# Performance work log

Measured on AMD Instinct MI355X. Metric: run time of the kernel, lower is better.

The kernel has to match this reference:

```python
import jax, jax.numpy as jnp
import numpy as np

NUM_EMB = 512
DIM = 65        # so dim-1 = 64 Householder reflections of size 64x64 per embedding
B, N = 2048, 256


def setup_inputs() -> dict:
    key = jax.random.key(0)
    k1, k2, k3, k4 = jax.random.split(key, 4)
    x = jax.random.normal(k1, (B, N, DIM), dtype=jnp.float32)
    r_idx = jax.random.randint(k2, (B,), 0, NUM_EMB)
    # learned params: embedding table and scalar flip_sign (nn.Parameter)
    emb_weight = jax.random.normal(k3, (NUM_EMB, (DIM - 1) * (DIM - 1)), dtype=jnp.float32)
    flip_sign = jax.random.normal(k4, (), dtype=jnp.float32)
    return {"x": x, "r_idx": r_idx, "emb_weight": emb_weight, "flip_sign": flip_sign}


def _flg_forward(x, emb_weight, flip_sign, r_idx):
    d = DIM - 1
    # GELU (exact, matching torch default) then view as [E, d, d]; row w is a reflection vector v
    v = jax.nn.gelu(emb_weight, approximate=False).reshape(NUM_EMB, d, d)
    # Householder matrices H[e, w] = I - 2 v v^T / (v . v)   -> [E, d, d, d]
    outer = jnp.einsum('ewv,ewk->ewvk', v, v)
    sqnorm = jnp.einsum('ewv,ewv->ew', v, v)[..., None, None]
    H = jnp.eye(d, dtype=x.dtype) - 2.0 * outer / sqnorm
    H = jnp.transpose(H, (1, 0, 2, 3))  # [d, E, d, d]: reflection index leading (scan axis)

    # sequential product W = I @ H[0] @ H[1] @ ... @ H[d-1], batched over E
    W0 = jnp.broadcast_to(jnp.eye(d, dtype=x.dtype), (NUM_EMB, d, d))
    def step(carry, Hi):
        return carry @ Hi, None
    W, _ = jax.lax.scan(step, W0, H)  # [E, d, d]

    # scale last column by flip_sign (in-place mul in torch)
    W = W.at[:, :, -1].multiply(flip_sign)

    Wb = W[r_idx]                        # [B, d, d]
    x0 = x[..., :1]                      # [B, N, 1]
    xn = jnp.einsum('bnd,bdc->bnc', x[..., 1:], Wb)  # rotate remaining coords
    return jnp.concatenate([x0, xn], axis=-1)


def reference(x, r_idx, emb_weight, flip_sign):
    xo = _flg_forward(x, emb_weight, flip_sign, r_idx)
    return (xo, r_idx)
```

## Files before the change

### kernel.cpp

```cpp
#include <hip/hip_runtime.h>
#include <math.h>

#define NUM_EMB 512
#define DIMV 65
#define DD   64
#define BB   2048
#define NN   256
#define IMGF (16 * DIMV)

typedef short short8 __attribute__((ext_vector_type(8)));
typedef float f32x4  __attribute__((ext_vector_type(4)));
typedef float f4u    __attribute__((ext_vector_type(4), aligned(4)));

__device__ __forceinline__ float gelu_exact(float x) {
    return 0.5f * x * (1.0f + erff(x * 0.7071067811865475f));
}

__device__ __forceinline__ unsigned f2bf_u(float f) {
    unsigned u = __builtin_bit_cast(unsigned, f);
    u += 0x7FFFu + ((u >> 16) & 1u);
    return u >> 16;
}
__device__ __forceinline__ unsigned short f2bf(float f) {
    return (unsigned short)f2bf_u(f);
}

__global__ __launch_bounds__(256) void build_W(const float* __restrict__ emb,
                                               const float* __restrict__ flip_sign,
                                               const int*   __restrict__ r_idx,
                                               unsigned short* __restrict__ WgT,
                                               float* __restrict__ out) {
    __shared__ float v_lds[DD * DD];
    __shared__ float s_lds[DD];
    const int e = blockIdx.x;
    const int t = threadIdx.x;
    const int r = t >> 2;
    const int q = t & 3;

    const float* erow = emb + (size_t)e * (DD * DD);
    #pragma unroll
    for (int p = 0; p < 16; ++p) {
        int idx = p * 256 + t;
        v_lds[idx] = gelu_exact(erow[idx]);
    }

    if (t < 4) {
        int bi = e * 4 + t;
        out[(size_t)BB * NN * DIMV + bi] = (float)r_idx[bi];
    }
    __syncthreads();

    {
        const float* vr = &v_lds[r * DD + q * 16];
        float ss = 0.f;
        #pragma unroll
        for (int k = 0; k < 16; ++k) ss += vr[k] * vr[k];
        ss += __shfl_xor(ss, 1);
        ss += __shfl_xor(ss, 2);
        if (q == 0) s_lds[r] = 2.0f / ss;
    }
    __syncthreads();

    float Wq[16];
    #pragma unroll
    for (int k = 0; k < 16; ++k) Wq[k] = ((q * 16 + k) == r) ? 1.0f : 0.0f;

    float vv[16], nv[16];
    {
        const float* vr = &v_lds[q * 16];
        *(float4*)&nv[0]  = *(const float4*)&vr[0];
        *(float4*)&nv[4]  = *(const float4*)&vr[4];
        *(float4*)&nv[8]  = *(const float4*)&vr[8];
        *(float4*)&nv[12] = *(const float4*)&vr[12];
    }

    for (int w = 0; w < DD; ++w) {
        #pragma unroll
        for (int k = 0; k < 16; ++k) vv[k] = nv[k];
        if (w < DD - 1) {
            const float* vr = &v_lds[(w + 1) * DD + q * 16];
            *(float4*)&nv[0]  = *(const float4*)&vr[0];
            *(float4*)&nv[4]  = *(const float4*)&vr[4];
            *(float4*)&nv[8]  = *(const float4*)&vr[8];
            *(float4*)&nv[12] = *(const float4*)&vr[12];
        }
        float p0 = Wq[0] * vv[0],  p1 = Wq[1] * vv[1];
        float p2 = Wq[2] * vv[2],  p3 = Wq[3] * vv[3];
        #pragma unroll
        for (int k = 4; k < 16; k += 4) {
            p0 += Wq[k]     * vv[k];
            p1 += Wq[k + 1] * vv[k + 1];
            p2 += Wq[k + 2] * vv[k + 2];
            p3 += Wq[k + 3] * vv[k + 3];
        }
        float p = (p0 + p1) + (p2 + p3);
        p += __shfl_xor(p, 1);
        p += __shfl_xor(p, 2);
        const float sc = s_lds[w] * p;
        #pragma unroll
        for (int k = 0; k < 16; ++k) Wq[k] -= sc * vv[k];
    }

    if (q == 3) Wq[15] *= flip_sign[0];

    unsigned short* wd = WgT + (size_t)e * (DD * DD) + r;
    #pragma unroll
    for (int k = 0; k < 16; ++k)
        wd[(16 * q + k) * DD] = f2bf(Wq[k]);
}

__global__ __launch_bounds__(256) void apply_W(const float* __restrict__ x,
                                               const int*   __restrict__ r_idx,
                                               const unsigned short* __restrict__ WgT,
                                               float* __restrict__ out) {
    __shared__ alignas(16) float IMG[4][IMGF];
    const int t = threadIdx.x;
    const int w = t >> 6;
    const int l = t & 63;
    const int lrow  = l & 15;
    const int kslot = l >> 4;

    const int gw = blockIdx.x * 4 + w;
    const size_t row0 = (size_t)gw * 64;
    const int b = gw >> 2;

    const int e = r_idx[b];
    float* img = IMG[w];

    const unsigned short* wb = WgT + (size_t)e * (DD * DD);
    short8 bfrg[4][2];
    #pragma unroll
    for (int ct = 0; ct < 4; ++ct)
        #pragma unroll
        for (int kb = 0; kb < 2; ++kb)
            bfrg[ct][kb] = *(const short8*)(wb + (ct * 16 + lrow) * DD + kb * 32 + kslot * 8);

    f4u   av[4][4];
    float x0v[4];
    #pragma unroll
    for (int i = 0; i < 4; ++i) {
        const float* xr = x + (row0 + i * 16 + lrow) * DIMV + 1 + kslot * 8;
        av[i][0] = *(const f4u*)(xr);
        av[i][1] = *(const f4u*)(xr + 4);
        av[i][2] = *(const f4u*)(xr + 32);
        av[i][3] = *(const f4u*)(xr + 36);
        x0v[i] = (l < 16) ? x[(row0 + i * 16 + l) * DIMV] : 0.f;
    }
    __builtin_amdgcn_sched_barrier(0);

    #pragma unroll
    for (int i = 0; i < 4; ++i) {
        short8 afrg[2];
        #pragma unroll
        for (int kb = 0; kb < 2; ++kb) {
            union { short8 s; unsigned u[4]; } af;
            const f4u a0 = av[i][kb * 2 + 0];
            const f4u a1 = av[i][kb * 2 + 1];
            af.u[0] = f2bf_u(a0.x) | (f2bf_u(a0.y) << 16);
            af.u[1] = f2bf_u(a0.z) | (f2bf_u(a0.w) << 16);
            af.u[2] = f2bf_u(a1.x) | (f2bf_u(a1.y) << 16);
            af.u[3] = f2bf_u(a1.z) | (f2bf_u(a1.w) << 16);
            afrg[kb] = af.s;
        }

        f32x4 acc[4];
        #pragma unroll
        for (int ct = 0; ct < 4; ++ct) {
            f32x4 c0 = {0.f, 0.f, 0.f, 0.f};
            c0 = __builtin_amdgcn_mfma_f32_16x16x32_bf16(afrg[0], bfrg[ct][0], c0, 0, 0, 0);
            c0 = __builtin_amdgcn_mfma_f32_16x16x32_bf16(afrg[1], bfrg[ct][1], c0, 0, 0, 0);
            acc[ct] = c0;
        }

        #pragma unroll
        for (int ct = 0; ct < 4; ++ct)
            #pragma unroll
            for (int rg = 0; rg < 4; ++rg)
                img[(kslot * 4 + rg) * DIMV + 1 + ct * 16 + lrow] = acc[ct][rg];
        if (l < 16) img[l * DIMV] = x0v[i];

        asm volatile("s_waitcnt lgkmcnt(0)" ::: "memory");
        __builtin_amdgcn_sched_barrier(0);

        {
            float4* og = (float4*)(out + (row0 + i * 16) * DIMV);
            const float4* iv = (const float4*)img;
            #pragma unroll
            for (int p = 0; p < 4; ++p) og[p * 64 + l] = iv[p * 64 + l];
            if (l < 4) og[256 + l] = iv[256 + l];
        }
    }
}

extern "C" void kernel_launch(void* const* d_in, const int* in_sizes, int n_in,
                              void* d_out, int out_size, void* d_ws, size_t ws_size,
                              hipStream_t stream) {
    const float* x         = (const float*)d_in[0];
    const int*   r_idx     = (const int*)d_in[1];
    const float* emb       = (const float*)d_in[2];
    const float* flip_sign = (const float*)d_in[3];
    float* out = (float*)d_out;
    unsigned short* WgT = (unsigned short*)d_ws;

    build_W<<<NUM_EMB, 256, 0, stream>>>(emb, flip_sign, r_idx, WgT, out);
    apply_W<<<BB, 256, 0, stream>>>(x, r_idx, WgT, out);
}
```

Before: 79.54 us.

## Double-buffer x tiles into LDS via direct global-to-LDS loads

The apply kernel now copies x tiles straight into LDS with global_load_lds, double-buffered, instead of unaligned float4 loads into registers. Explicit vmcnt waits overlap the load of the next tile with compute and stores for the current one. Each wave now processes 128 rows (8 tiles), and the grid is halved to match. Column 0 of x now passes through in the LDS image instead of being loaded separately. The risks are larger LDS use per block and hand-counted vmcnt values that depend on stores also being counted in vmcnt.

```diff
diff --git a/kernel.cpp b/kernel.cpp
--- a/kernel.cpp
+++ b/kernel.cpp
@@ -6,11 +6,12 @@
 #define DD   64
 #define BB   2048
 #define NN   256
-#define IMGF (16 * DIMV)
+#define TILEF 1040
+#define WTILES 8
+#define GRID_APPLY ((BB * NN) / (128 * 4))
 
 typedef short short8 __attribute__((ext_vector_type(8)));
 typedef float f32x4  __attribute__((ext_vector_type(4)));
-typedef float f4u    __attribute__((ext_vector_type(4), aligned(4)));
 
 __device__ __forceinline__ float gelu_exact(float x) {
     return 0.5f * x * (1.0f + erff(x * 0.7071067811865475f));
@@ -113,19 +114,21 @@
                                                const int*   __restrict__ r_idx,
                                                const unsigned short* __restrict__ WgT,
                                                float* __restrict__ out) {
-    __shared__ alignas(16) float IMG[4][IMGF];
+    __shared__ alignas(16) float IMG[4][2 * TILEF];
     const int t = threadIdx.x;
     const int w = t >> 6;
     const int l = t & 63;
     const int lrow  = l & 15;
     const int kslot = l >> 4;
 
-    const int gw = blockIdx.x * 4 + w;
-    const size_t row0 = (size_t)gw * 64;
-    const int b = gw >> 2;
+    const int    gw   = blockIdx.x * 4 + w;
+    const size_t row0 = (size_t)gw * 128;
+    const int    b    = gw >> 1;
 
     const int e = r_idx[b];
     float* img = IMG[w];
+    const float* xw = x   + row0 * DIMV;
+    float*       ow = out + row0 * DIMV;
 
     const unsigned short* wb = WgT + (size_t)e * (DD * DD);
     short8 bfrg[4][2];
@@ -135,31 +138,27 @@
         for (int kb = 0; kb < 2; ++kb)
             bfrg[ct][kb] = *(const short8*)(wb + (ct * 16 + lrow) * DD + kb * 32 + kslot * 8);
 
-    f4u   av[4][4];
-    float x0v[4];
-    #pragma unroll
-    for (int i = 0; i < 4; ++i) {
-        const float* xr = x + (row0 + i * 16 + lrow) * DIMV + 1 + kslot * 8;
-        av[i][0] = *(const f4u*)(xr);
-        av[i][1] = *(const f4u*)(xr + 4);
-        av[i][2] = *(const f4u*)(xr + 32);
-        av[i][3] = *(const f4u*)(xr + 36);
-        x0v[i] = (l < 16) ? x[(row0 + i * 16 + l) * DIMV] : 0.f;
-    }
-    __builtin_amdgcn_sched_barrier(0);
-
-    #pragma unroll
-    for (int i = 0; i < 4; ++i) {
+    auto issue_loads = [&](int i) {
+        const float* g = xw + (size_t)i * TILEF;
+        float* d = img + (i & 1) * TILEF;
+        __builtin_amdgcn_global_load_lds((const unsigned*)(g + 0   + 4 * l), (unsigned*)(d + 0),    16, 0, 0);
+        __builtin_amdgcn_global_load_lds((const unsigned*)(g + 256 + 4 * l), (unsigned*)(d + 256),  16, 0, 0);
+        __builtin_amdgcn_global_load_lds((const unsigned*)(g + 512 + 4 * l), (unsigned*)(d + 512),  16, 0, 0);
+        __builtin_amdgcn_global_load_lds((const unsigned*)(g + 768 + 4 * l), (unsigned*)(d + 768),  16, 0, 0);
+        if (l < 4)
+            __builtin_amdgcn_global_load_lds((const unsigned*)(g + 1024 + 4 * l), (unsigned*)(d + 1024), 16, 0, 0);
+    };
+
+    auto do_tile = [&](int i) {
+        const float* buf = img + (i & 1) * TILEF;
         short8 afrg[2];
         #pragma unroll
         for (int kb = 0; kb < 2; ++kb) {
+            const float* xp = buf + lrow * DIMV + 1 + kb * 32 + kslot * 8;
             union { short8 s; unsigned u[4]; } af;
-            const f4u a0 = av[i][kb * 2 + 0];
-            const f4u a1 = av[i][kb * 2 + 1];
-            af.u[0] = f2bf_u(a0.x) | (f2bf_u(a0.y) << 16);
-            af.u[1] = f2bf_u(a0.z) | (f2bf_u(a0.w) << 16);
-            af.u[2] = f2bf_u(a1.x) | (f2bf_u(a1.y) << 16);
-            af.u[3] = f2bf_u(a1.z) | (f2bf_u(a1.w) << 16);
+            #pragma unroll
+            for (int jj = 0; jj < 4; ++jj)
+                af.u[jj] = f2bf_u(xp[2 * jj]) | (f2bf_u(xp[2 * jj + 1]) << 16);
             afrg[kb] = af.s;
         }
 
@@ -172,24 +171,42 @@
             acc[ct] = c0;
         }
 
+        float* bufw = img + (i & 1) * TILEF;
         #pragma unroll
         for (int ct = 0; ct < 4; ++ct)
             #pragma unroll
             for (int rg = 0; rg < 4; ++rg)
-                img[(kslot * 4 + rg) * DIMV + 1 + ct * 16 + lrow] = acc[ct][rg];
-        if (l < 16) img[l * DIMV] = x0v[i];
-
-        asm volatile("s_waitcnt lgkmcnt(0)" ::: "memory");
-        __builtin_amdgcn_sched_barrier(0);
-
-        {
-            float4* og = (float4*)(out + (row0 + i * 16) * DIMV);
-            const float4* iv = (const float4*)img;
-            #pragma unroll
-            for (int p = 0; p < 4; ++p) og[p * 64 + l] = iv[p * 64 + l];
-            if (l < 4) og[256 + l] = iv[256 + l];
-        }
-    }
+                bufw[(kslot * 4 + rg) * DIMV + 1 + ct * 16 + lrow] = acc[ct][rg];
+
+        float4* og = (float4*)(ow + (size_t)i * TILEF);
+        const float4* iv = (const float4*)bufw;
+        #pragma unroll
+        for (int p = 0; p < 4; ++p) og[p * 64 + l] = iv[p * 64 + l];
+        if (l < 4) og[256 + l] = iv[256 + l];
+    };
+
+    issue_loads(0);
+    issue_loads(1);
+    __builtin_amdgcn_sched_barrier(0);
+
+#define TILE_STEP(I, VMSTR)                                   \
+    do {                                                      \
+        if ((I) + 1 < WTILES) issue_loads((I) + 1);           \
+        __builtin_amdgcn_sched_barrier(0);                    \
+        asm volatile("s_waitcnt " VMSTR ::: "memory");        \
+        __builtin_amdgcn_sched_barrier(0);                    \
+        do_tile(I);                                           \
+    } while (0)
+
+    TILE_STEP(0, "vmcnt(5)");
+    TILE_STEP(1, "vmcnt(10)");
+    TILE_STEP(2, "vmcnt(10)");
+    TILE_STEP(3, "vmcnt(10)");
+    TILE_STEP(4, "vmcnt(10)");
+    TILE_STEP(5, "vmcnt(10)");
+    TILE_STEP(6, "vmcnt(10)");
+    TILE_STEP(7, "vmcnt(5)");
+#undef TILE_STEP
 }
 
 extern "C" void kernel_launch(void* const* d_in, const int* in_sizes, int n_in,
@@ -203,5 +220,5 @@
     unsigned short* WgT = (unsigned short*)d_ws;
 
     build_W<<<NUM_EMB, 256, 0, stream>>>(emb, flip_sign, r_idx, WgT, out);
-    apply_W<<<BB, 256, 0, stream>>>(x, r_idx, WgT, out);
-}
+    apply_W<<<GRID_APPLY, 256, 0, stream>>>(x, r_idx, WgT, out);
+}
```

Result: no change. 78.17 us (-1.7%).
